# Optimization experiments

Measured on AMD Instinct MI355X. Metric: run time of the kernel, lower is better.

The kernel has to match this reference:

```python
import jax, jax.numpy as jnp
import numpy as np

H = 32  # hidden_size


def _lstm_scan(x_tbd, Wih, Whh, b):
    # Single-direction LSTM. x_tbd: [T,B,D]; Wih: [4H,D]; Whh: [4H,H]; b: [4H]
    B = x_tbd.shape[1]
    h0 = jnp.zeros((B, Whh.shape[1]), x_tbd.dtype)
    c0 = h0
    xW = jnp.einsum('tbd,gd->tbg', x_tbd, Wih) + b  # precompute input projection [T,B,4H]

    def step(carry, xw):
        h, c = carry
        g = xw + h @ Whh.T
        i, f, gg, o = jnp.split(g, 4, axis=-1)  # PyTorch gate order i,f,g,o
        c = jax.nn.sigmoid(f) * c + jax.nn.sigmoid(i) * jnp.tanh(gg)
        h = jax.nn.sigmoid(o) * jnp.tanh(c)
        return (h, c), h

    _, hs = jax.lax.scan(step, (h0, c0), xW)
    return hs  # [T,B,H]


def _bilstm_layer(x_btd, Wih, Whh, b):
    # x_btd: [B,T,D]; Wih: [2,4H,D] (dir 0 = fwd, 1 = bwd)
    xt = x_btd.transpose(1, 0, 2)
    hf = _lstm_scan(xt, Wih[0], Whh[0], b[0])
    hb = _lstm_scan(xt[::-1], Wih[1], Whh[1], b[1])[::-1]
    return jnp.concatenate([hf, hb], -1).transpose(1, 0, 2)  # [B,T,2H]


def _bilstm(x, Wih0, Whh0, b0, Wih1, Whh1, b1):
    x = _bilstm_layer(x, Wih0, Whh0, b0)
    x = _bilstm_layer(x, Wih1, Whh1, b1)
    return x[:, -1, :]  # [B,2H] (fwd final state | bwd state at last position)


def setup_inputs() -> dict:
    key = jax.random.key(0)
    ks = jax.random.split(key, 20)
    B, T, D = 32768, 30, 4
    k = 1.0 / np.sqrt(H)

    def u(kk, shape):
        return jax.random.uniform(kk, shape, jnp.float32, -k, k)

    inp = {
        'dir_input': jax.random.normal(ks[0], (B, 6), jnp.float32),
        'position_input': jax.random.normal(ks[1], (B, T, D), jnp.float32),
    }
    # lvl and vor bidirectional 2-layer LSTMs; b = b_ih + b_hh combined
    for i, name in enumerate(['lvl', 'vor']):
        o = 2 + i * 6
        inp[name + '_Wih0'] = u(ks[o + 0], (2, 4 * H, D))
        inp[name + '_Whh0'] = u(ks[o + 1], (2, 4 * H, H))
        inp[name + '_b0'] = u(ks[o + 2], (2, 4 * H))
        inp[name + '_Wih1'] = u(ks[o + 3], (2, 4 * H, 2 * H))
        inp[name + '_Whh1'] = u(ks[o + 4], (2, 4 * H, H))
        inp[name + '_b1'] = u(ks[o + 5], (2, 4 * H))
    inp['lvl_fc_W'] = u(ks[14], (2, 2 * H))
    inp['lvl_fc_b'] = u(ks[15], (2,))
    inp['vor_fc_W'] = u(ks[16], (2, 4 * H))
    inp['vor_fc_b'] = u(ks[17], (2,))
    return inp


def reference(dir_input, position_input,
              lvl_Wih0, lvl_Whh0, lvl_b0, lvl_Wih1, lvl_Whh1, lvl_b1,
              vor_Wih0, vor_Whh0, vor_b0, vor_Wih1, vor_Whh1, vor_b1,
              lvl_fc_W, lvl_fc_b, vor_fc_W, vor_fc_b):
    P = 15  # position_len
    dirs = jnp.argmax(dir_input, axis=1)
    dt = position_input.dtype
    mask_vor = ((dirs == 1) | (dirs == 4)).astype(dt)[:, None]
    mask_r = ((dirs == 0) | (dirs == 5)).astype(dt)[:, None]
    mask_l = ((dirs == 2) | (dirs == 3)).astype(dt)[:, None]

    # Batch left/right halves through one LSTM call per branch (same weights)
    halves = jnp.concatenate([position_input[:, :P, :], position_input[:, P:, :]], axis=0)

    lvl_last = _bilstm(halves, lvl_Wih0, lvl_Whh0, lvl_b0, lvl_Wih1, lvl_Whh1, lvl_b1)
    lvl_l, lvl_r = jnp.split(lvl_last, 2, axis=0)
    # dropout is identity in eval mode
    x_r = (lvl_r @ lvl_fc_W.T + lvl_fc_b) * mask_r
    x_l = (lvl_l @ lvl_fc_W.T + lvl_fc_b) * mask_l

    vor_last = _bilstm(halves, vor_Wih0, vor_Whh0, vor_b0, vor_Wih1, vor_Whh1, vor_b1)
    vor_l, vor_r = jnp.split(vor_last, 2, axis=0)
    x_vor = (jnp.concatenate([vor_l, vor_r], axis=1) @ vor_fc_W.T + vor_fc_b) * mask_vor

    return x_r + x_l + x_vor
```

## Files before the change

### kernel.cpp

```cpp
#include <hip/hip_runtime.h>
#include <hip/hip_bf16.h>

typedef _Float16 f16x8 __attribute__((ext_vector_type(8)));
typedef _Float16 f16x4 __attribute__((ext_vector_type(4)));
typedef float    f32x4 __attribute__((ext_vector_type(4)));

#define LOG2E  1.44269504f
#define LOG2E2 2.88539008f

#define HIST_TILE_HALFS 15360
#define LL_OFF_B 62390272
#define LV_OFF_B 62521344
#define CT_OFF_B 62783488

__device__ __forceinline__ float cellT(float fi, float ff, float fg, float fo, float& c) {
    float ei = __builtin_amdgcn_exp2f(fi);
    float ef = __builtin_amdgcn_exp2f(ff);
    float eg = __builtin_amdgcn_exp2f(fg);
    float A  = 1.0f + ef;
    float B  = 1.0f + ei;
    float C  = 1.0f + eg;
    float Cm2 = eg - 1.0f;
    float BC = B * C;
    float cn = fmaf(c, BC, A * Cm2) * __builtin_amdgcn_rcpf(A * BC);
    c = cn;
    float eo = __builtin_amdgcn_exp2f(fo);
    float ec = __builtin_amdgcn_exp2f(LOG2E2 * cn);
    return (ec - 1.0f) * __builtin_amdgcn_rcpf((1.0f + eo) * (1.0f + ec));
}

__device__ __forceinline__ f16x8 afrag8(const float* __restrict__ p, float s) {
    const float4 w0 = *(const float4*)p;
    const float4 w1 = *(const float4*)(p + 4);
    f16x8 v;
    v[0] = (_Float16)(w0.x * s); v[1] = (_Float16)(w0.y * s);
    v[2] = (_Float16)(w0.z * s); v[3] = (_Float16)(w0.w * s);
    v[4] = (_Float16)(w1.x * s); v[5] = (_Float16)(w1.y * s);
    v[6] = (_Float16)(w1.z * s); v[7] = (_Float16)(w1.w * s);
    return v;
}

__device__ __forceinline__ float gscale(int nb) {
    return ((nb >> 1) == 2) ? LOG2E2 : -LOG2E;
}

__device__ __forceinline__ int jperm(int nb, int m) {
    return 8 * (m >> 2) + 4 * (nb & 1) + (m & 3);
}

#define HAVE_K16 __has_builtin(__builtin_amdgcn_mfma_f32_16x16x16f16)

__global__ __launch_bounds__(256) void k0_cls(
    const float* __restrict__ dir_input,
    int* __restrict__ list_lvl, int* __restrict__ list_vor,
    int* __restrict__ cnts)
{
    const int b    = blockIdx.x * 256 + threadIdx.x;
    const int lane = threadIdx.x & 63;

    const float* dp = dir_input + (size_t)b * 6;
    float mx = dp[0];
    int dmax = 0;
#pragma unroll
    for (int i = 1; i < 6; ++i) {
        const float v = dp[i];
        if (v > mx) { mx = v; dmax = i; }
    }
    const bool isv = (dmax == 1) || (dmax == 4);
    const int  hf  = (dmax == 0 || dmax == 5) ? 1 : 0;

    {
        const unsigned long long mk = __ballot(!isv);
        const int n = __popcll(mk);
        if (n) {
            const int leader = __ffsll((unsigned long long)mk) - 1;
            int base = 0;
            if (lane == leader) base = atomicAdd(&cnts[0], n);
            base = __shfl(base, leader);
            if (!isv) {
                const int rank = __popcll(mk & ((1ull << lane) - 1ull));
                list_lvl[base + rank] = b | (hf << 15);
            }
        }
    }
    {
        const unsigned long long mv = __ballot(isv);
        const int n = __popcll(mv);
        if (n) {
            const int leader = __ffsll((unsigned long long)mv) - 1;
            int base = 0;
            if (lane == leader) base = atomicAdd(&cnts[1], 2 * n);
            base = __shfl(base, leader);
            if (isv) {
                const int rank = __popcll(mv & ((1ull << lane) - 1ull));
                list_vor[base + 2 * rank]     = b;
                list_vor[base + 2 * rank + 1] = b | (1 << 15);
            }
        }
    }
}

__global__ __launch_bounds__(256, 4) void k1_l0(
    const float* __restrict__ pos,
    const float* __restrict__ lvl_Wih0, const float* __restrict__ lvl_Whh0,
    const float* __restrict__ lvl_b0,
    const float* __restrict__ vor_Wih0, const float* __restrict__ vor_Whh0,
    const float* __restrict__ vor_b0,
    _Float16* __restrict__ hist,
    const int* __restrict__ list_lvl, const int* __restrict__ list_vor,
    const int* __restrict__ cnts)
{
    const int lane = threadIdx.x & 63;
    const int wv   = threadIdx.x >> 6;
    const int n0   = lane & 15;
    const int quad = lane >> 4;
    const int tile = blockIdx.x * 4 + wv;
    const int m    = blockIdx.y >> 1;
    const int dir  = blockIdx.y & 1;

    const int cnt = cnts[m];
    if (tile * 16 >= cnt) return;

    const int* list = m ? list_vor : list_lvl;
    const int  li   = tile * 16 + n0;
    const int  e    = (li < cnt) ? list[li] : 0;
    const int  b    = e & 32767;
    const int  hf   = (e >> 15) & 1;

    const float* Wih = (m ? vor_Wih0 : lvl_Wih0) + dir * 128 * 4;
    const float* Whh = (m ? vor_Whh0 : lvl_Whh0) + dir * 128 * 32;
    const float* bs  = (m ? vor_b0   : lvl_b0)   + dir * 128;

    f16x8 WhhA[8];
#if HAVE_K16
    f16x4 WihA[8];
#else
    f16x8 WihA[8];
#endif
#pragma unroll
    for (int nb = 0; nb < 8; ++nb) {
        const int J = (nb >> 1) * 32 + jperm(nb, n0);
        const float s = gscale(nb);
        WhhA[nb] = afrag8(Whh + J * 32 + quad * 8, s);
#if HAVE_K16
        f16x4 v = {(_Float16)0.0f, (_Float16)0.0f, (_Float16)0.0f, (_Float16)0.0f};
        if (quad == 0) {
            const float4 w = *(const float4*)(Wih + J * 4);
            v[0] = (_Float16)(w.x * s); v[1] = (_Float16)(w.y * s);
            v[2] = (_Float16)(w.z * s); v[3] = (_Float16)(w.w * s);
        } else if (quad == 1) {
            v[0] = (_Float16)(bs[J] * s);
        }
        WihA[nb] = v;
#else
        f16x8 v;
#pragma unroll
        for (int r = 0; r < 8; ++r) v[r] = (_Float16)0.0f;
        if (quad == 0) {
            const float4 w = *(const float4*)(Wih + J * 4);
            v[0] = (_Float16)(w.x * s); v[1] = (_Float16)(w.y * s);
            v[2] = (_Float16)(w.z * s); v[3] = (_Float16)(w.w * s);
            v[4] = (_Float16)(bs[J] * s);
        }
        WihA[nb] = v;
#endif
    }

    const float* xp = pos + ((size_t)b * 30 + hf * 15 + (dir ? 14 : 0)) * 4;
    const int xstep = dir ? -4 : 4;

    _Float16* hp = hist + ((size_t)(m * 2048 + tile)) * HIST_TILE_HALFS
                 + (size_t)(dir ? 14 : 0) * 1024 + dir * 512 + lane * 8;
    const int hstep = dir ? -1024 : 1024;

    float c[4][2];
#pragma unroll
    for (int r = 0; r < 4; ++r) { c[r][0] = 0.0f; c[r][1] = 0.0f; }

    f16x8 hB;
#pragma unroll
    for (int r = 0; r < 8; ++r) hB[r] = (_Float16)0.0f;

    const f32x4 z4 = {0.0f, 0.0f, 0.0f, 0.0f};

    float4 xn  = *(const float4*)xp;
    float4 xn2 = *(const float4*)(xp + xstep);

#pragma unroll 3
    for (int ti = 0; ti < 15; ++ti) {
        const float4 xv = xn;
        xn = xn2;
        const int tn2 = (ti < 13) ? (ti + 2) : 14;
        xn2 = *(const float4*)(xp + tn2 * xstep);

#if HAVE_K16
        f16x4 xB = {(_Float16)0.0f, (_Float16)0.0f, (_Float16)0.0f, (_Float16)0.0f};
        if (quad == 0) {
            xB[0] = (_Float16)xv.x; xB[1] = (_Float16)xv.y;
            xB[2] = (_Float16)xv.z; xB[3] = (_Float16)xv.w;
        } else if (quad == 1) {
            xB[0] = (_Float16)1.0f;
        }
#else
        f16x8 xB;
#pragma unroll
        for (int r = 0; r < 8; ++r) xB[r] = (_Float16)0.0f;
        if (quad == 0) {
            xB[0] = (_Float16)xv.x; xB[1] = (_Float16)xv.y;
            xB[2] = (_Float16)xv.z; xB[3] = (_Float16)xv.w;
            xB[4] = (_Float16)1.0f;
        }
#endif

        f32x4 acc[8];
#pragma unroll
        for (int nb = 0; nb < 8; ++nb)
#if HAVE_K16
            acc[nb] = __builtin_amdgcn_mfma_f32_16x16x16f16(WihA[nb], xB, z4, 0, 0, 0);
#else
            acc[nb] = __builtin_amdgcn_mfma_f32_16x16x32_f16(WihA[nb], xB, z4, 0, 0, 0);
#endif
#pragma unroll
        for (int nb = 0; nb < 8; ++nb)
            acc[nb] = __builtin_amdgcn_mfma_f32_16x16x32_f16(WhhA[nb], hB, acc[nb], 0, 0, 0);

        f16x8 nh;
#pragma unroll
        for (int r = 0; r < 4; ++r) {
            nh[r]     = (_Float16)cellT(acc[0][r], acc[2][r], acc[4][r], acc[6][r], c[r][0]);
            nh[4 + r] = (_Float16)cellT(acc[1][r], acc[3][r], acc[5][r], acc[7][r], c[r][1]);
        }
        hB = nh;

        *(f16x8*)hp = hB;
        hp += hstep;
    }
}

__global__ __launch_bounds__(256, 2) void k2_l1(
    const float* __restrict__ lvl_Wih1, const float* __restrict__ lvl_Whh1,
    const float* __restrict__ lvl_b1,
    const float* __restrict__ vor_Wih1, const float* __restrict__ vor_Whh1,
    const float* __restrict__ vor_b1,
    const float* __restrict__ lvl_fc_W, const float* __restrict__ lvl_fc_b,
    const float* __restrict__ vor_fc_W, const float* __restrict__ vor_fc_b,
    const _Float16* __restrict__ hist, float* __restrict__ out,
    const int* __restrict__ list_lvl, const int* __restrict__ list_vor,
    const int* __restrict__ cnts)
{
    const int lane  = threadIdx.x & 63;
    const int wv    = threadIdx.x >> 6;
    const int n0    = lane & 15;
    const int quad  = lane >> 4;
    const int tpair = (blockIdx.x * 4 + wv) * 2;
    const int m     = blockIdx.y;

    const float* Wih = m ? vor_Wih1 : lvl_Wih1;
    const float* Whh = m ? vor_Whh1 : lvl_Whh1;
    const float* bs  = m ? vor_b1   : lvl_b1;

    __shared__ __align__(16) _Float16 whlds[8 * 64 * 8];
    __shared__ __align__(16) float    blds[8 * 64 * 4];

    if (threadIdx.x < 64) {
#pragma unroll
        for (int nb = 0; nb < 8; ++nb) {
            const int g = nb >> 1, p = nb & 1;
            const int J = g * 32 + jperm(nb, n0);
            const float s = gscale(nb);
            *(f16x8*)(whlds + ((size_t)nb * 64 + lane) * 8) = afrag8(Whh + J * 32 + quad * 8, s);
            const float4 bq = *(const float4*)(bs + g * 32 + 8 * quad + 4 * p);
            f32x4 bv; bv[0] = bq.x * s; bv[1] = bq.y * s; bv[2] = bq.z * s; bv[3] = bq.w * s;
            *(f32x4*)(blds + ((size_t)nb * 64 + lane) * 4) = bv;
        }
    }

    const int cnt = cnts[m];
    const bool active = (tpair * 16 < cnt);
    const int* list = m ? list_vor : list_lvl;

    f16x8 WA[8], WB[8];
    if (active) {
#pragma unroll
        for (int nb = 0; nb < 8; ++nb) {
            const int J = (nb >> 1) * 32 + jperm(nb, n0);
            const float s = gscale(nb);
            WA[nb] = afrag8(Wih + J * 64 + quad * 8, s);
            WB[nb] = afrag8(Wih + J * 64 + 32 + quad * 8, s);
        }
    }
    __syncthreads();
    if (!active) return;

    const _Float16* hb[2];
#pragma unroll
    for (int tt = 0; tt < 2; ++tt)
        hb[tt] = hist + ((size_t)(m * 2048 + tpair + tt)) * HIST_TILE_HALFS + lane * 8;

    float c1[2][4][2];
#pragma unroll
    for (int tt = 0; tt < 2; ++tt)
#pragma unroll
        for (int r = 0; r < 4; ++r) { c1[tt][r][0] = 0.0f; c1[tt][r][1] = 0.0f; }
    f16x8 h1B[2];
#pragma unroll
    for (int tt = 0; tt < 2; ++tt)
#pragma unroll
        for (int r = 0; r < 8; ++r) h1B[tt][r] = (_Float16)0.0f;
    float h1f_a[2][4], h1f_b[2][4];
    f16x8 a_f[2], a_b[2];

    f16x8 nf0[2], nb0[2], nf1[2], nb1[2];
#pragma unroll
    for (int tt = 0; tt < 2; ++tt) {
        nf0[tt] = *(const f16x8*)(hb[tt]);
        nb0[tt] = *(const f16x8*)(hb[tt] + 512);
        nf1[tt] = *(const f16x8*)(hb[tt] + 1024);
        nb1[tt] = *(const f16x8*)(hb[tt] + 1024 + 512);
    }

#pragma unroll 1
    for (int t = 0; t < 15; ++t) {
#pragma unroll
        for (int tt = 0; tt < 2; ++tt) {
            a_f[tt] = nf0[tt]; a_b[tt] = nb0[tt];
            nf0[tt] = nf1[tt]; nb0[tt] = nb1[tt];
        }
        const int tn2 = (t < 13) ? (t + 2) : 14;
#pragma unroll
        for (int tt = 0; tt < 2; ++tt) {
            nf1[tt] = *(const f16x8*)(hb[tt] + (size_t)tn2 * 1024);
            nb1[tt] = *(const f16x8*)(hb[tt] + (size_t)tn2 * 1024 + 512);
        }

#pragma unroll
        for (int tt = 0; tt < 2; ++tt) {
            f32x4 acc[8];
#pragma unroll
            for (int nb = 0; nb < 8; ++nb) {
                const f32x4 bv = *(const f32x4*)(blds + ((size_t)nb * 64 + lane) * 4);
                acc[nb] = __builtin_amdgcn_mfma_f32_16x16x32_f16(WA[nb], a_f[tt], bv, 0, 0, 0);
            }
#pragma unroll
            for (int nb = 0; nb < 8; ++nb)
                acc[nb] = __builtin_amdgcn_mfma_f32_16x16x32_f16(WB[nb], a_b[tt], acc[nb], 0, 0, 0);
#pragma unroll
            for (int nb = 0; nb < 8; ++nb) {
                const f16x8 wh = *(const f16x8*)(whlds + ((size_t)nb * 64 + lane) * 8);
                acc[nb] = __builtin_amdgcn_mfma_f32_16x16x32_f16(wh, h1B[tt], acc[nb], 0, 0, 0);
            }

            f16x8 nh;
#pragma unroll
            for (int r = 0; r < 4; ++r) {
                float ha  = cellT(acc[0][r], acc[2][r], acc[4][r], acc[6][r], c1[tt][r][0]);
                float hbv = cellT(acc[1][r], acc[3][r], acc[5][r], acc[7][r], c1[tt][r][1]);
                h1f_a[tt][r] = ha; h1f_b[tt][r] = hbv;
                nh[r] = (_Float16)ha; nh[4 + r] = (_Float16)hbv;
            }
            h1B[tt] = nh;
        }
    }

    float h1b_a[2][4], h1b_b[2][4];
    {
        const float* Wb = Wih + 128 * 64;
        const float* bb = bs + 128;
        const int nbs[6] = {0, 1, 4, 5, 6, 7};
        f32x4 accb[2][6];
#pragma unroll
        for (int q6 = 0; q6 < 6; ++q6) {
            const int nb = nbs[q6];
            const int g = nb >> 1, p = nb & 1;
            const int J = g * 32 + jperm(nb, n0);
            const float s = gscale(nb);
            const f16x8 wa = afrag8(Wb + J * 64 + quad * 8, s);
            const f16x8 wb = afrag8(Wb + J * 64 + 32 + quad * 8, s);
            const float4 bq = *(const float4*)(bb + g * 32 + 8 * quad + 4 * p);
            f32x4 bv; bv[0] = bq.x * s; bv[1] = bq.y * s; bv[2] = bq.z * s; bv[3] = bq.w * s;
#pragma unroll
            for (int tt = 0; tt < 2; ++tt) {
                f32x4 a = __builtin_amdgcn_mfma_f32_16x16x32_f16(wa, a_f[tt], bv, 0, 0, 0);
                a = __builtin_amdgcn_mfma_f32_16x16x32_f16(wb, a_b[tt], a, 0, 0, 0);
                accb[tt][q6] = a;
            }
        }
#pragma unroll
        for (int tt = 0; tt < 2; ++tt)
#pragma unroll
            for (int r = 0; r < 4; ++r) {
#pragma unroll
                for (int p = 0; p < 2; ++p) {
                    const float i_ = accb[tt][0 + p][r];
                    const float g_ = accb[tt][2 + p][r];
                    const float o_ = accb[tt][4 + p][r];
                    float ei = __builtin_amdgcn_exp2f(i_);
                    float eg = __builtin_amdgcn_exp2f(g_);
                    float Bv = 1.0f + ei;
                    float C  = 1.0f + eg;
                    float cv = (eg - 1.0f) * __builtin_amdgcn_rcpf(Bv * C);
                    float eo = __builtin_amdgcn_exp2f(o_);
                    float ec = __builtin_amdgcn_exp2f(LOG2E2 * cv);
                    float h = (ec - 1.0f) * __builtin_amdgcn_rcpf((1.0f + eo) * (1.0f + ec));
                    if (p == 0) h1b_a[tt][r] = h; else h1b_b[tt][r] = h;
                }
            }
    }

#pragma unroll
    for (int tt = 0; tt < 2; ++tt) {
        const int  li    = (tpair + tt) * 16 + n0;
        const bool valid = li < cnt;
        const int  e     = valid ? list[li] : 0;
        const int  b     = e & 32767;
        const int  hf    = (e >> 15) & 1;

        float pr[2];
#pragma unroll
        for (int o = 0; o < 2; ++o) {
            const float* Wr = (m == 0) ? (lvl_fc_W + o * 64)
                                       : (vor_fc_W + o * 128 + hf * 64);
            const float4 wfa = *(const float4*)(Wr + 8 * quad);
            const float4 wfb = *(const float4*)(Wr + 8 * quad + 4);
            const float4 wba = *(const float4*)(Wr + 32 + 8 * quad);
            const float4 wbb = *(const float4*)(Wr + 32 + 8 * quad + 4);
            float a = wfa.x * h1f_a[tt][0] + wfa.y * h1f_a[tt][1]
                    + wfa.z * h1f_a[tt][2] + wfa.w * h1f_a[tt][3];
            a += wfb.x * h1f_b[tt][0] + wfb.y * h1f_b[tt][1]
               + wfb.z * h1f_b[tt][2] + wfb.w * h1f_b[tt][3];
            a += wba.x * h1b_a[tt][0] + wba.y * h1b_a[tt][1]
               + wba.z * h1b_a[tt][2] + wba.w * h1b_a[tt][3];
            a += wbb.x * h1b_b[tt][0] + wbb.y * h1b_b[tt][1]
               + wbb.z * h1b_b[tt][2] + wbb.w * h1b_b[tt][3];
            pr[o] = a;
        }
#pragma unroll
        for (int o = 0; o < 2; ++o) {
            pr[o] += __shfl_xor(pr[o], 16);
            pr[o] += __shfl_xor(pr[o], 32);
        }

        float r0 = pr[0], r1 = pr[1];
        if (m == 1) {
            r0 += __shfl_xor(pr[0], 1);
            r1 += __shfl_xor(pr[1], 1);
        }

        if (quad == 0 && valid && (m == 0 || (n0 & 1) == 0)) {
            const float b0v = m ? vor_fc_b[0] : lvl_fc_b[0];
            const float b1v = m ? vor_fc_b[1] : lvl_fc_b[1];
            float2 o2; o2.x = r0 + b0v; o2.y = r1 + b1v;
            *(float2*)(out + (size_t)b * 2) = o2;
        }
    }
}

extern "C" void kernel_launch(void* const* d_in, const int* in_sizes, int n_in,
                              void* d_out, int out_size, void* d_ws, size_t ws_size,
                              hipStream_t stream) {
    const float* dir_input = (const float*)d_in[0];
    const float* pos       = (const float*)d_in[1];
    const float* lvl_Wih0  = (const float*)d_in[2];
    const float* lvl_Whh0  = (const float*)d_in[3];
    const float* lvl_b0    = (const float*)d_in[4];
    const float* lvl_Wih1  = (const float*)d_in[5];
    const float* lvl_Whh1  = (const float*)d_in[6];
    const float* lvl_b1    = (const float*)d_in[7];
    const float* vor_Wih0  = (const float*)d_in[8];
    const float* vor_Whh0  = (const float*)d_in[9];
    const float* vor_b0    = (const float*)d_in[10];
    const float* vor_Wih1  = (const float*)d_in[11];
    const float* vor_Whh1  = (const float*)d_in[12];
    const float* vor_b1    = (const float*)d_in[13];
    const float* lvl_fc_W  = (const float*)d_in[14];
    const float* lvl_fc_b  = (const float*)d_in[15];
    const float* vor_fc_W  = (const float*)d_in[16];
    const float* vor_fc_b  = (const float*)d_in[17];
    float* out = (float*)d_out;
    _Float16* hist = (_Float16*)d_ws;
    char* wsb = (char*)d_ws;

    int* list_lvl = (int*)(wsb + LL_OFF_B);
    int* list_vor = (int*)(wsb + LV_OFF_B);
    int* cnts     = (int*)(wsb + CT_OFF_B);

    (void)in_sizes; (void)n_in; (void)ws_size; (void)out_size;

    hipMemsetAsync(cnts, 0, 2 * sizeof(int), stream);

    dim3 blk(256, 1, 1);
    hipLaunchKernelGGL(k0_cls, dim3(128, 1, 1), blk, 0, stream,
                       dir_input, list_lvl, list_vor, cnts);

    hipLaunchKernelGGL(k1_l0, dim3(512, 4, 1), blk, 0, stream,
                       pos, lvl_Wih0, lvl_Whh0, lvl_b0,
                       vor_Wih0, vor_Whh0, vor_b0,
                       hist, list_lvl, list_vor, cnts);

    hipLaunchKernelGGL(k2_l1, dim3(256, 2, 1), blk, 0, stream,
                       lvl_Wih1, lvl_Whh1, lvl_b1,
                       vor_Wih1, vor_Whh1, vor_b1,
                       lvl_fc_W, lvl_fc_b, vor_fc_W, vor_fc_b,
                       hist, out, list_lvl, list_vor, cnts);
}
```

Before: 217.2 us.

## Process one tile per wave in layer-1 kernel and stage Wih in LDS

The layer-1 LSTM kernel now handles a single 16-sequence tile per wave instead of two interleaved tiles, and doubles the grid to cover the same work. Input-weight fragments move from per-wave registers into shared memory alongside the recurrent weights. Together these cut register pressure and add waves for latency hiding. The cost is losing the two-tile interleave that hid MFMA and transcendental latency within a wave, plus extra LDS reads on every step.

```diff
diff --git a/kernel.cpp b/kernel.cpp
--- a/kernel.cpp
+++ b/kernel.cpp
@@ -248,18 +248,18 @@
     const int* __restrict__ list_lvl, const int* __restrict__ list_vor,
     const int* __restrict__ cnts)
 {
-    const int lane  = threadIdx.x & 63;
-    const int wv    = threadIdx.x >> 6;
-    const int n0    = lane & 15;
-    const int quad  = lane >> 4;
-    const int tpair = (blockIdx.x * 4 + wv) * 2;
-    const int m     = blockIdx.y;
+    const int lane = threadIdx.x & 63;
+    const int wv   = threadIdx.x >> 6;
+    const int n0   = lane & 15;
+    const int quad = lane >> 4;
+    const int tile = blockIdx.x * 4 + wv;
+    const int m    = blockIdx.y;
 
     const float* Wih = m ? vor_Wih1 : lvl_Wih1;
     const float* Whh = m ? vor_Whh1 : lvl_Whh1;
     const float* bs  = m ? vor_b1   : lvl_b1;
 
-    __shared__ __align__(16) _Float16 whlds[8 * 64 * 8];
+    __shared__ __align__(16) _Float16 wlds[24 * 64 * 8];
     __shared__ __align__(16) float    blds[8 * 64 * 4];
 
     if (threadIdx.x < 64) {
@@ -268,106 +268,79 @@
             const int g = nb >> 1, p = nb & 1;
             const int J = g * 32 + jperm(nb, n0);
             const float s = gscale(nb);
-            *(f16x8*)(whlds + ((size_t)nb * 64 + lane) * 8) = afrag8(Whh + J * 32 + quad * 8, s);
+            *(f16x8*)(wlds + ((size_t)(nb)      * 64 + lane) * 8) = afrag8(Wih + J * 64 + quad * 8, s);
+            *(f16x8*)(wlds + ((size_t)(8 + nb)  * 64 + lane) * 8) = afrag8(Wih + J * 64 + 32 + quad * 8, s);
+            *(f16x8*)(wlds + ((size_t)(16 + nb) * 64 + lane) * 8) = afrag8(Whh + J * 32 + quad * 8, s);
             const float4 bq = *(const float4*)(bs + g * 32 + 8 * quad + 4 * p);
             f32x4 bv; bv[0] = bq.x * s; bv[1] = bq.y * s; bv[2] = bq.z * s; bv[3] = bq.w * s;
             *(f32x4*)(blds + ((size_t)nb * 64 + lane) * 4) = bv;
         }
     }
+    __syncthreads();
 
     const int cnt = cnts[m];
-    const bool active = (tpair * 16 < cnt);
+    if (tile * 16 >= cnt) return;
     const int* list = m ? list_vor : list_lvl;
 
-    f16x8 WA[8], WB[8];
-    if (active) {
-#pragma unroll
-        for (int nb = 0; nb < 8; ++nb) {
-            const int J = (nb >> 1) * 32 + jperm(nb, n0);
-            const float s = gscale(nb);
-            WA[nb] = afrag8(Wih + J * 64 + quad * 8, s);
-            WB[nb] = afrag8(Wih + J * 64 + 32 + quad * 8, s);
-        }
-    }
-    __syncthreads();
-    if (!active) return;
-
-    const _Float16* hb[2];
-#pragma unroll
-    for (int tt = 0; tt < 2; ++tt)
-        hb[tt] = hist + ((size_t)(m * 2048 + tpair + tt)) * HIST_TILE_HALFS + lane * 8;
-
-    float c1[2][4][2];
-#pragma unroll
-    for (int tt = 0; tt < 2; ++tt)
-#pragma unroll
-        for (int r = 0; r < 4; ++r) { c1[tt][r][0] = 0.0f; c1[tt][r][1] = 0.0f; }
-    f16x8 h1B[2];
-#pragma unroll
-    for (int tt = 0; tt < 2; ++tt)
-#pragma unroll
-        for (int r = 0; r < 8; ++r) h1B[tt][r] = (_Float16)0.0f;
-    float h1f_a[2][4], h1f_b[2][4];
-    f16x8 a_f[2], a_b[2];
-
-    f16x8 nf0[2], nb0[2], nf1[2], nb1[2];
-#pragma unroll
-    for (int tt = 0; tt < 2; ++tt) {
-        nf0[tt] = *(const f16x8*)(hb[tt]);
-        nb0[tt] = *(const f16x8*)(hb[tt] + 512);
-        nf1[tt] = *(const f16x8*)(hb[tt] + 1024);
-        nb1[tt] = *(const f16x8*)(hb[tt] + 1024 + 512);
-    }
+    const _Float16* hbp = hist + ((size_t)(m * 2048 + tile)) * HIST_TILE_HALFS + lane * 8;
+
+    float c1[4][2];
+#pragma unroll
+    for (int r = 0; r < 4; ++r) { c1[r][0] = 0.0f; c1[r][1] = 0.0f; }
+    f16x8 h1B;
+#pragma unroll
+    for (int r = 0; r < 8; ++r) h1B[r] = (_Float16)0.0f;
+    float h1f_a[4], h1f_b[4];
+    f16x8 a_f, a_b;
+
+    f16x8 nf0 = *(const f16x8*)(hbp);
+    f16x8 nb0 = *(const f16x8*)(hbp + 512);
+    f16x8 nf1 = *(const f16x8*)(hbp + 1024);
+    f16x8 nb1 = *(const f16x8*)(hbp + 1024 + 512);
 
 #pragma unroll 1
     for (int t = 0; t < 15; ++t) {
-#pragma unroll
-        for (int tt = 0; tt < 2; ++tt) {
-            a_f[tt] = nf0[tt]; a_b[tt] = nb0[tt];
-            nf0[tt] = nf1[tt]; nb0[tt] = nb1[tt];
-        }
+        a_f = nf0; a_b = nb0;
+        nf0 = nf1; nb0 = nb1;
         const int tn2 = (t < 13) ? (t + 2) : 14;
-#pragma unroll
-        for (int tt = 0; tt < 2; ++tt) {
-            nf1[tt] = *(const f16x8*)(hb[tt] + (size_t)tn2 * 1024);
-            nb1[tt] = *(const f16x8*)(hb[tt] + (size_t)tn2 * 1024 + 512);
-        }
-
-#pragma unroll
-        for (int tt = 0; tt < 2; ++tt) {
-            f32x4 acc[8];
-#pragma unroll
-            for (int nb = 0; nb < 8; ++nb) {
-                const f32x4 bv = *(const f32x4*)(blds + ((size_t)nb * 64 + lane) * 4);
-                acc[nb] = __builtin_amdgcn_mfma_f32_16x16x32_f16(WA[nb], a_f[tt], bv, 0, 0, 0);
-            }
-#pragma unroll
-            for (int nb = 0; nb < 8; ++nb)
-                acc[nb] = __builtin_amdgcn_mfma_f32_16x16x32_f16(WB[nb], a_b[tt], acc[nb], 0, 0, 0);
-#pragma unroll
-            for (int nb = 0; nb < 8; ++nb) {
-                const f16x8 wh = *(const f16x8*)(whlds + ((size_t)nb * 64 + lane) * 8);
-                acc[nb] = __builtin_amdgcn_mfma_f32_16x16x32_f16(wh, h1B[tt], acc[nb], 0, 0, 0);
-            }
-
-            f16x8 nh;
-#pragma unroll
-            for (int r = 0; r < 4; ++r) {
-                float ha  = cellT(acc[0][r], acc[2][r], acc[4][r], acc[6][r], c1[tt][r][0]);
-                float hbv = cellT(acc[1][r], acc[3][r], acc[5][r], acc[7][r], c1[tt][r][1]);
-                h1f_a[tt][r] = ha; h1f_b[tt][r] = hbv;
-                nh[r] = (_Float16)ha; nh[4 + r] = (_Float16)hbv;
-            }
-            h1B[tt] = nh;
-        }
-    }
-
-    float h1b_a[2][4], h1b_b[2][4];
+        nf1 = *(const f16x8*)(hbp + (size_t)tn2 * 1024);
+        nb1 = *(const f16x8*)(hbp + (size_t)tn2 * 1024 + 512);
+
+        f32x4 acc[8];
+#pragma unroll
+        for (int nb = 0; nb < 8; ++nb) {
+            const f16x8 wa = *(const f16x8*)(wlds + ((size_t)nb * 64 + lane) * 8);
+            const f32x4 bv = *(const f32x4*)(blds + ((size_t)nb * 64 + lane) * 4);
+            acc[nb] = __builtin_amdgcn_mfma_f32_16x16x32_f16(wa, a_f, bv, 0, 0, 0);
+        }
+#pragma unroll
+        for (int nb = 0; nb < 8; ++nb) {
+            const f16x8 wb = *(const f16x8*)(wlds + ((size_t)(8 + nb) * 64 + lane) * 8);
+            acc[nb] = __builtin_amdgcn_mfma_f32_16x16x32_f16(wb, a_b, acc[nb], 0, 0, 0);
+        }
+#pragma unroll
+        for (int nb = 0; nb < 8; ++nb) {
+            const f16x8 wh = *(const f16x8*)(wlds + ((size_t)(16 + nb) * 64 + lane) * 8);
+            acc[nb] = __builtin_amdgcn_mfma_f32_16x16x32_f16(wh, h1B, acc[nb], 0, 0, 0);
+        }
+
+        f16x8 nh;
+#pragma unroll
+        for (int r = 0; r < 4; ++r) {
+            float ha  = cellT(acc[0][r], acc[2][r], acc[4][r], acc[6][r], c1[r][0]);
+            float hbv = cellT(acc[1][r], acc[3][r], acc[5][r], acc[7][r], c1[r][1]);
+            h1f_a[r] = ha; h1f_b[r] = hbv;
+            nh[r] = (_Float16)ha; nh[4 + r] = (_Float16)hbv;
+        }
+        h1B = nh;
+    }
+
+    float h1b_a[4], h1b_b[4];
     {
         const float* Wb = Wih + 128 * 64;
         const float* bb = bs + 128;
         const int nbs[6] = {0, 1, 4, 5, 6, 7};
-        f32x4 accb[2][6];
+        f32x4 accb[6];
 #pragma unroll
         for (int q6 = 0; q6 < 6; ++q6) {
             const int nb = nbs[q6];
@@ -378,38 +351,32 @@
             const f16x8 wb = afrag8(Wb + J * 64 + 32 + quad * 8, s);
             const float4 bq = *(const float4*)(bb + g * 32 + 8 * quad + 4 * p);
             f32x4 bv; bv[0] = bq.x * s; bv[1] = bq.y * s; bv[2] = bq.z * s; bv[3] = bq.w * s;
-#pragma unroll
-            for (int tt = 0; tt < 2; ++tt) {
-                f32x4 a = __builtin_amdgcn_mfma_f32_16x16x32_f16(wa, a_f[tt], bv, 0, 0, 0);
-                a = __builtin_amdgcn_mfma_f32_16x16x32_f16(wb, a_b[tt], a, 0, 0, 0);
-                accb[tt][q6] = a;
+            f32x4 a = __builtin_amdgcn_mfma_f32_16x16x32_f16(wa, a_f, bv, 0, 0, 0);
+            a = __builtin_amdgcn_mfma_f32_16x16x32_f16(wb, a_b, a, 0, 0, 0);
+            accb[q6] = a;
+        }
+#pragma unroll
+        for (int r = 0; r < 4; ++r) {
+#pragma unroll
+            for (int p = 0; p < 2; ++p) {
+                const float i_ = accb[0 + p][r];
+                const float g_ = accb[2 + p][r];
+                const float o_ = accb[4 + p][r];
+                float ei = __builtin_amdgcn_exp2f(i_);
+                float eg = __builtin_amdgcn_exp2f(g_);
+                float Bv = 1.0f + ei;
+                float C  = 1.0f + eg;
+                float cv = (eg - 1.0f) * __builtin_amdgcn_rcpf(Bv * C);
+                float eo = __builtin_amdgcn_exp2f(o_);
+                float ec = __builtin_amdgcn_exp2f(LOG2E2 * cv);
+                float h = (ec - 1.0f) * __builtin_amdgcn_rcpf((1.0f + eo) * (1.0f + ec));
+                if (p == 0) h1b_a[r] = h; else h1b_b[r] = h;
             }
         }
-#pragma unroll
-        for (int tt = 0; tt < 2; ++tt)
-#pragma unroll
-            for (int r = 0; r < 4; ++r) {
-#pragma unroll
-                for (int p = 0; p < 2; ++p) {
-                    const float i_ = accb[tt][0 + p][r];
-                    const float g_ = accb[tt][2 + p][r];
-                    const float o_ = accb[tt][4 + p][r];
-                    float ei = __builtin_amdgcn_exp2f(i_);
-                    float eg = __builtin_amdgcn_exp2f(g_);
-                    float Bv = 1.0f + ei;
-                    float C  = 1.0f + eg;
-                    float cv = (eg - 1.0f) * __builtin_amdgcn_rcpf(Bv * C);
-                    float eo = __builtin_amdgcn_exp2f(o_);
-                    float ec = __builtin_amdgcn_exp2f(LOG2E2 * cv);
-                    float h = (ec - 1.0f) * __builtin_amdgcn_rcpf((1.0f + eo) * (1.0f + ec));
-                    if (p == 0) h1b_a[tt][r] = h; else h1b_b[tt][r] = h;
-                }
-            }
-    }
-
-#pragma unroll
-    for (int tt = 0; tt < 2; ++tt) {
-        const int  li    = (tpair + tt) * 16 + n0;
+    }
+
+    {
+        const int  li    = tile * 16 + n0;
         const bool valid = li < cnt;
         const int  e     = valid ? list[li] : 0;
         const int  b     = e & 32767;
@@ -424,14 +391,14 @@
             const float4 wfb = *(const float4*)(Wr + 8 * quad + 4);
             const float4 wba = *(const float4*)(Wr + 32 + 8 * quad);
             const float4 wbb = *(const float4*)(Wr + 32 + 8 * quad + 4);
-            float a = wfa.x * h1f_a[tt][0] + wfa.y * h1f_a[tt][1]
-                    + wfa.z * h1f_a[tt][2] + wfa.w * h1f_a[tt][3];
-            a += wfb.x * h1f_b[tt][0] + wfb.y * h1f_b[tt][1]
-               + wfb.z * h1f_b[tt][2] + wfb.w * h1f_b[tt][3];
-            a += wba.x * h1b_a[tt][0] + wba.y * h1b_a[tt][1]
-               + wba.z * h1b_a[tt][2] + wba.w * h1b_a[tt][3];
-            a += wbb.x * h1b_b[tt][0] + wbb.y * h1b_b[tt][1]
-               + wbb.z * h1b_b[tt][2] + wbb.w * h1b_b[tt][3];
+            float a = wfa.x * h1f_a[0] + wfa.y * h1f_a[1]
+                    + wfa.z * h1f_a[2] + wfa.w * h1f_a[3];
+            a += wfb.x * h1f_b[0] + wfb.y * h1f_b[1]
+               + wfb.z * h1f_b[2] + wfb.w * h1f_b[3];
+            a += wba.x * h1b_a[0] + wba.y * h1b_a[1]
+               + wba.z * h1b_a[2] + wba.w * h1b_a[3];
+            a += wbb.x * h1b_b[0] + wbb.y * h1b_b[1]
+               + wbb.z * h1b_b[2] + wbb.w * h1b_b[3];
             pr[o] = a;
         }
 #pragma unroll
@@ -497,7 +464,7 @@
                        vor_Wih0, vor_Whh0, vor_b0,
                        hist, list_lvl, list_vor, cnts);
 
-    hipLaunchKernelGGL(k2_l1, dim3(256, 2, 1), blk, 0, stream,
+    hipLaunchKernelGGL(k2_l1, dim3(512, 2, 1), blk, 0, stream,
                        lvl_Wih1, lvl_Whh1, lvl_b1,
                        vor_Wih1, vor_Whh1, vor_b1,
                        lvl_fc_W, lvl_fc_b, vor_fc_W, vor_fc_b,
```

Measured after the change: 212.6 us. 2.1% less time.
